# Performance work log

Measured on AMD Instinct MI355X. Metric: run time of the kernel, lower is better.

Reference implementation:

```python
import jax, jax.numpy as jnp
import numpy as np
from jax import lax

RO = 4.0            # snake_config.ro (feature-map downsample ratio)
N_ADJ = 4           # snake_config.adj_num -> kernel = 2*4+1 = 9
K = 2 * N_ADJ + 1
DIL = (1, 1, 1, 2, 2, 4, 4)   # dilations of the 7 Snake residual circular convs
NMS_RADIUS = 2      # radius used in the iterative refinement cls_nms


def circ_conv(x, w, b, d):
    """Dilated circular conv along polygon axis. x:[N,C,P], w:[O,I,K]."""
    pad = N_ADJ * d
    xp = jnp.concatenate([x[..., -pad:], x, x[..., :pad]], axis=-1)
    y = lax.conv_general_dilated(xp, w, window_strides=(1,), padding='VALID',
                                 rhs_dilation=(d,),
                                 dimension_numbers=('NCH', 'OIH', 'NCH'))
    return y + b[None, :, None]


def conv1x1(x, w, b):
    # x:[N,C,P], w:[O,C] -> [N,O,P]
    return jnp.einsum('ncp,oc->nop', x, w) + b[None, :, None]


def bilinear_gather(cnn_feature, poly, ind):
    """grid_sample-style bilinear sampling (align_corners=False, zero pad).
    cnn_feature:[B,C,H,W], poly:[N,P,2] pixel coords, ind:[N] image index.
    Returns [N,C,P]."""
    B, C, H, W = cnn_feature.shape
    x = poly[..., 0] - 0.5
    y = poly[..., 1] - 0.5
    x0 = jnp.floor(x); y0 = jnp.floor(y)
    wx = x - x0; wy = y - y0
    x0i = x0.astype(jnp.int32); y0i = y0.astype(jnp.int32)

    def tap(yi, xi):
        valid = (xi >= 0) & (xi < W) & (yi >= 0) & (yi < H)
        xi_c = jnp.clip(xi, 0, W - 1)
        yi_c = jnp.clip(yi, 0, H - 1)
        f = cnn_feature[ind[:, None], :, yi_c, xi_c]  # [N,P,C]
        return f * valid[..., None]

    f00 = tap(y0i, x0i);     f01 = tap(y0i, x0i + 1)
    f10 = tap(y0i + 1, x0i); f11 = tap(y0i + 1, x0i + 1)
    out = (f00 * ((1 - wx) * (1 - wy))[..., None]
           + f01 * (wx * (1 - wy))[..., None]
           + f10 * ((1 - wx) * wy)[..., None]
           + f11 * (wx * wy)[..., None])
    return out.transpose(0, 2, 1)  # [N,C,P]


def cls_nms(cls, radius):
    """Circular local-max suppression of per-vertex scores. cls:[N,P,1]."""
    c = cls[..., 0]
    m = jnp.max(jnp.stack([jnp.roll(c, s, axis=1)
                           for s in range(-radius, radius + 1)], 0), axis=0)
    return jnp.where(c >= m, c, 0.0)[..., None]


def snake_body(x, head_w, head_b, res_w, res_b, fusion_w, fusion_b,
               pred1_w, pred1_b, pred2_w, pred2_b, pred3_w, pred3_b,
               cls1_w, cls1_b, cls2_w, cls2_b, cls3_w, cls3_b):
    h = jax.nn.relu(circ_conv(x, head_w, head_b, 1))
    states = [h]
    for i in range(7):  # fixed 7 residual layers, structurally distinct dilations
        r = jax.nn.relu(circ_conv(states[-1], res_w[i], res_b[i], DIL[i]))
        states.append(r + states[-1])
    state = jnp.concatenate(states, axis=1)                 # [N, 8*128, P]
    g = conv1x1(state, fusion_w, fusion_b)                  # [N, 256, P]
    g = jnp.max(g, axis=2, keepdims=True)
    g = jnp.broadcast_to(g, (state.shape[0], g.shape[1], state.shape[2]))
    state = jnp.concatenate([g, state], axis=1)             # [N, 1280, P]

    def head3(w1, b1, w2, b2, w3, b3):
        h1 = jax.nn.relu(conv1x1(state, w1, b1))
        h2 = jax.nn.relu(conv1x1(h1, w2, b2))
        return conv1x1(h2, w3, b3)

    offset = head3(pred1_w, pred1_b, pred2_w, pred2_b, pred3_w, pred3_b)  # [N,2,P]
    cls = head3(cls1_w, cls1_b, cls2_w, cls2_b, cls3_w, cls3_b)           # [N,1,P]
    return offset, cls


def setup_inputs() -> dict:
    key = jax.random.key(0)
    ks = jax.random.split(key, 32)
    B, C, H, W = 4, 64, 128, 128
    N, P = 512, 128
    SD = 128  # state_dim
    FD = 64 + 2 + 1  # feature_dim for iterative evolve_gcn
    std = 0.01  # conv init: normal(0, 0.01), bias 0 (matches module init)
    inp = {
        'cnn_feature': jax.random.normal(ks[0], (B, C, H, W), jnp.float32),
        'i_it_py': jax.random.uniform(ks[1], (N, P, 2), jnp.float32) * (W - 1),
        'c_it_py': jax.random.normal(ks[2], (N, P, 2), jnp.float32) * 0.2,
        'it_cls': jax.random.uniform(ks[3], (N, P), jnp.float32),
        'ind': jax.random.randint(ks[4], (N,), 0, B, jnp.int32),
        'head_w': jax.random.normal(ks[5], (SD, FD, K), jnp.float32) * std,
        'head_b': jnp.zeros((SD,), jnp.float32),
        'res_w': jax.random.normal(ks[6], (7, SD, SD, K), jnp.float32) * std,
        'res_b': jnp.zeros((7, SD), jnp.float32),
        'fusion_w': jax.random.normal(ks[7], (256, 8 * SD), jnp.float32) * std,
        'fusion_b': jnp.zeros((256,), jnp.float32),
        'pred1_w': jax.random.normal(ks[8], (256, 8 * SD + 256), jnp.float32) * std,
        'pred1_b': jnp.zeros((256,), jnp.float32),
        'pred2_w': jax.random.normal(ks[9], (64, 256), jnp.float32) * std,
        'pred2_b': jnp.zeros((64,), jnp.float32),
        'pred3_w': jax.random.normal(ks[10], (2, 64), jnp.float32) * std,
        'pred3_b': jnp.zeros((2,), jnp.float32),
        'cls1_w': jax.random.normal(ks[11], (256, 8 * SD + 256), jnp.float32) * std,
        'cls1_b': jnp.zeros((256,), jnp.float32),
        'cls2_w': jax.random.normal(ks[12], (64, 256), jnp.float32) * std,
        'cls2_b': jnp.zeros((64,), jnp.float32),
        'cls3_w': jax.random.normal(ks[13], (1, 64), jnp.float32) * std,
        'cls3_b': jnp.zeros((1,), jnp.float32),
    }
    return inp


def reference(cnn_feature, i_it_py, c_it_py, it_cls, ind,
              head_w, head_b, res_w, res_b, fusion_w, fusion_b,
              pred1_w, pred1_b, pred2_w, pred2_b, pred3_w, pred3_b,
              cls1_w, cls1_b, cls2_w, cls2_b, cls3_w, cls3_b):
    # evolve_poly: gather CNN features at vertices, concat scaled canonical
    # coords + per-vertex cls, run Snake, add offsets, NMS sigmoid scores.
    feat = bilinear_gather(cnn_feature, i_it_py, ind)        # [N,64,P]
    c = (c_it_py * RO).transpose(0, 2, 1)                    # [N,2,P]
    x = jnp.concatenate([feat, c, it_cls[:, None, :]], axis=1)  # [N,67,P]
    offset, cls = snake_body(x, head_w, head_b, res_w, res_b, fusion_w, fusion_b,
                             pred1_w, pred1_b, pred2_w, pred2_b, pred3_w, pred3_b,
                             cls1_w, cls1_b, cls2_w, cls2_b, cls3_w, cls3_b)
    i_poly = i_it_py * RO + offset.transpose(0, 2, 1)        # [N,P,2]
    cls = cls.transpose(0, 2, 1)                             # [N,P,1]
    nms = cls_nms(jax.nn.sigmoid(cls), NMS_RADIUS)           # [N,P,1]
    return i_poly, cls, nms
```

## Files before the change

kernel.cpp:

```cpp
#include <hip/hip_runtime.h>
#include <math.h>

typedef __attribute__((ext_vector_type(8))) short bf16x8;
typedef __attribute__((ext_vector_type(4))) float f32x4;

#define UOFF_CAW 0L
#define UOFF_FAW 2359296L
#define UOFF_H1W 2883584L
#define UOFF_W2F 3932160L
#define NB_TOT   3997696L
#define OFF_W1G  1998848L
#define OFF_GRAW 2129920L
#define OFF_DYN  2260992L
#define REPACK_N 4128768L

__device__ inline ushort f2bf_rne(float x) {
  uint u = __float_as_uint(x);
  return (ushort)((u + 0x7FFFu + ((u >> 16) & 1u)) >> 16);
}
__device__ inline void split_bf(float x, ushort& h, ushort& l) {
  uint u = __float_as_uint(x);
  uint hb = (u + 0x7FFFu + ((u >> 16) & 1u)) & 0xFFFF0000u;
  h = (ushort)(hb >> 16);
  l = f2bf_rne(x - __uint_as_float(hb));
}
__device__ inline ushort bfsel(float w, int split) {
  uint u = __float_as_uint(w);
  uint hb = (u + 0x7FFFu + ((u >> 16) & 1u)) & 0xFFFF0000u;
  if (split == 0) return (ushort)(hb >> 16);
  float lo = w - __uint_as_float(hb);
  uint ul = __float_as_uint(lo);
  return (ushort)((ul + 0x7FFFu + ((ul >> 16) & 1u)) >> 16);
}
__device__ inline bf16x8 asb(uint4 a) {
  union { uint4 u; bf16x8 v; } x; x.u = a; return x.v;
}
__device__ inline f32x4 MFMA_(bf16x8 a, bf16x8 b, f32x4 c) {
  return __builtin_amdgcn_mfma_f32_16x16x32_bf16(a, b, c, 0, 0, 0);
}
__device__ inline void bar_lgkm() {
  asm volatile("s_waitcnt lgkmcnt(0)" ::: "memory");
  __builtin_amdgcn_s_barrier();
}

__device__ inline void read_frag_pair(const char* xb, int pc, int g, int ic,
                                      bf16x8& bh, bf16x8& bl) {
  const int s0 = (pc & 7) << 4;
  const char* a = xb + pc * 512 + (((ic * 64 + (g << 4))) ^ s0);
  bh = asb(*(const uint4*)a);
  bl = asb(*(const uint4*)(a + 256));
}

__global__ void k_repack(const float* __restrict__ head_w, const float* __restrict__ res_w,
                         const float* __restrict__ fusion_w,
                         const float* __restrict__ pred1_w, const float* __restrict__ cls1_w,
                         const float* __restrict__ pred2_w, const float* __restrict__ cls2_w,
                         float* __restrict__ ws) {
  const long j = (long)blockIdx.x * 256 + threadIdx.x;
  if (j >= REPACK_N) return;
  if (j < NB_TOT) {
    ushort* wsu = (ushort*)ws;
    float w;
    if (j < UOFF_FAW) {
      int e = (int)(j & 7); long q = j >> 3;
      int lane = (int)(q & 63); q >>= 6;
      int mt = (int)(q & 1); q >>= 1;
      int split = (int)(q & 1); q >>= 1;
      int ic = (int)(q & 3); q >>= 2;
      int tap = (int)(q % 9); q /= 9;
      int mp = (int)(q & 3); int l = (int)(q >> 2);
      int gg = lane >> 4;
      int kl = (e < 4) ? (4 * gg + e) : (16 + 4 * gg + e - 4);
      int m = mp * 32 + mt * 16 + (lane & 15);
      int i = ic * 32 + kl;
      if (l == 0) w = (i < 67) ? head_w[((long)m * 67 + i) * 9 + tap] : 0.f;
      else        w = res_w[(((long)(l - 1) * 128 + m) * 128 + i) * 9 + tap];
      wsu[j] = bfsel(w, split);
    } else if (j < UOFF_H1W) {
      long jj = j - UOFF_FAW;
      int e = (int)(jj & 7); long q = jj >> 3;
      int lane = (int)(q & 63); q >>= 6;
      int mt = (int)(q & 1); q >>= 1;
      int split = (int)(q & 1); q >>= 1;
      int ic = (int)(q & 3); q >>= 2;
      int fm2 = (int)(q & 7); int l = (int)(q >> 3);
      int gg = lane >> 4;
      int kl = (e < 4) ? (4 * gg + e) : (16 + 4 * gg + e - 4);
      int m = fm2 * 32 + mt * 16 + (lane & 15);
      int i = ic * 32 + kl;
      w = fusion_w[(long)m * 1024 + l * 128 + i];
      wsu[j] = bfsel(w, split);
    } else if (j < UOFF_W2F) {
      long jj = j - UOFF_H1W;
      int e = (int)(jj & 7); long q = jj >> 3;
      int lane = (int)(q & 63); q >>= 6;
      int mt = (int)(q & 1); q >>= 1;
      int split = (int)(q & 1); q >>= 1;
      int ic = (int)(q & 3); q >>= 2;
      int slab = (int)(q & 7); q >>= 3;
      int mp = (int)(q & 7); int blk = (int)(q >> 3);
      int gg = lane >> 4;
      int kl = (e < 4) ? (4 * gg + e) : (16 + 4 * gg + e - 4);
      int m = blk * 256 + mp * 32 + mt * 16 + (lane & 15);
      int k = slab * 128 + ic * 32 + kl;
      w = (m < 256) ? pred1_w[(long)m * 1280 + 256 + k] : cls1_w[(long)(m - 256) * 1280 + 256 + k];
      wsu[j] = bfsel(w, split);
    } else {
      long jj = j - UOFF_W2F;
      int e = (int)(jj & 7); long q = jj >> 3;
      int lane = (int)(q & 63); q >>= 6;
      int split = (int)(q & 1); q >>= 1;
      int ic = (int)(q & 7); q >>= 3;
      int mfr = (int)(q & 3); int blk = (int)(q >> 2);
      int gg = lane >> 4;
      int kl = (e < 4) ? (4 * gg + e) : (16 + 4 * gg + e - 4);
      int m = mfr * 16 + (lane & 15);
      int k = ic * 32 + kl;
      w = blk ? cls2_w[(long)m * 256 + k] : pred2_w[(long)m * 256 + k];
      wsu[j] = bfsel(w, split);
    }
  } else {
    long q = j - NB_TOT; int o = (int)(q & 511); int c = (int)(q >> 9);
    ws[OFF_W1G + q] = (o < 256) ? pred1_w[(long)o * 1280 + c] : cls1_w[(long)(o - 256) * 1280 + c];
  }
}

__global__ __launch_bounds__(1024) __attribute__((amdgpu_waves_per_eu(4)))
void k_conv(const float* __restrict__ cnn, const float* __restrict__ i_it,
            const float* __restrict__ c_it, const float* __restrict__ cls_in,
            const int* __restrict__ ind,
            const ushort* __restrict__ CAW, const ushort* __restrict__ FAW,
            const float* __restrict__ head_b, const float* __restrict__ res_b,
            float* __restrict__ graw, float* __restrict__ states, int p0) {
  __shared__ uint4 xt4[4096];
  __shared__ float scr[512];
  char* xb = (char*)xt4;
  const int ln = blockIdx.x, n = p0 + ln, t = threadIdx.x;
  const int lane = t & 63, li = lane & 15, g = lane >> 4;
  const int wv = __builtin_amdgcn_readfirstlane(t >> 6);
  const int mp = wv & 3, np = wv >> 2;
  const int fm2 = wv & 7, fq = wv >> 3;

  {
    const int p = t & 127, qg = t >> 7;
    const long nb = (long)n * 128 + p;
    const int sw = p & 7;
    if (qg < 4) {
      const float gx = i_it[nb * 2 + 0] - 0.5f;
      const float gy = i_it[nb * 2 + 1] - 0.5f;
      const float fx = floorf(gx), fy = floorf(gy);
      const float wx = gx - fx, wy = gy - fy;
      const int x0 = (int)fx, y0 = (int)fy, x1 = x0 + 1, y1 = y0 + 1;
      const bool vx0 = (x0 >= 0) & (x0 < 128), vx1 = (x1 >= 0) & (x1 < 128);
      const bool vy0 = (y0 >= 0) & (y0 < 128), vy1 = (y1 >= 0) & (y1 < 128);
      const int x0c = min(max(x0, 0), 127), x1c = min(max(x1, 0), 127);
      const int y0c = min(max(y0, 0), 127), y1c = min(max(y1, 0), 127);
      const float w00 = (vx0 && vy0) ? (1.f - wx) * (1.f - wy) : 0.f;
      const float w01 = (vx1 && vy0) ? wx * (1.f - wy) : 0.f;
      const float w10 = (vx0 && vy1) ? (1.f - wx) * wy : 0.f;
      const float w11 = (vx1 && vy1) ? wx * wy : 0.f;
      const long base = (long)ind[n] * (64L * 16384);
      const int a00 = y0c * 128 + x0c, a01 = y0c * 128 + x1c;
      const int a10 = y1c * 128 + x0c, a11 = y1c * 128 + x1c;
#pragma unroll
      for (int qq = 0; qq < 4; qq++) {
        ushort hh[4], ll[4];
#pragma unroll
        for (int cc = 0; cc < 4; cc++) {
          const int c = qg * 16 + qq * 4 + cc;
          const float* f = cnn + base + (long)c * 16384;
          float x = f[a00] * w00 + f[a01] * w01 + f[a10] * w10 + f[a11] * w11;
          split_bf(x, hh[cc], ll[cc]);
        }
        const int G = ((qg >> 1) * 4 + qq) ^ sw;
        char* a = xb + p * 512 + G * 16 + (qg & 1) * 8;
        *(uint2*)a = make_uint2((uint)hh[0] | ((uint)hh[1] << 16), (uint)hh[2] | ((uint)hh[3] << 16));
        *(uint2*)(a + 256) = make_uint2((uint)ll[0] | ((uint)ll[1] << 16), (uint)ll[2] | ((uint)ll[3] << 16));
      }
    } else {
#pragma unroll
      for (int qq = 0; qq < 4; qq++) {
        ushort hh[4], ll[4];
        if (qg == 4 && qq == 0) {
          float v0 = c_it[nb * 2 + 0] * 4.f, v1 = c_it[nb * 2 + 1] * 4.f, v2 = cls_in[nb];
          split_bf(v0, hh[0], ll[0]); split_bf(v1, hh[1], ll[1]); split_bf(v2, hh[2], ll[2]);
          hh[3] = 0; ll[3] = 0;
        } else {
          hh[0] = hh[1] = hh[2] = hh[3] = 0; ll[0] = ll[1] = ll[2] = ll[3] = 0;
        }
        const int G = ((qg >> 1) * 4 + qq) ^ sw;
        char* a = xb + p * 512 + G * 16 + (qg & 1) * 8;
        *(uint2*)a = make_uint2((uint)hh[0] | ((uint)hh[1] << 16), (uint)hh[2] | ((uint)hh[3] << 16));
        *(uint2*)(a + 256) = make_uint2((uint)ll[0] | ((uint)ll[1] << 16), (uint)ll[2] | ((uint)ll[3] << 16));
      }
    }
  }
  __syncthreads();

  const f32x4 fz = {0.f, 0.f, 0.f, 0.f};
  f32x4 facc[2][4];
#pragma unroll
  for (int a = 0; a < 2; a++)
#pragma unroll
    for (int b = 0; b < 4; b++) facc[a][b] = fz;

  const uint4* caw = (const uint4*)CAW;
  const uint4* faw = (const uint4*)FAW;
  uint4* stq = (uint4*)(states + (long)ln * 131072);

  for (int l = 0; l < 8; l++) {
    const int dil = (l >= 6) ? 4 : ((l >= 4) ? 2 : 1);
    const int nic = (l == 0) ? 3 : 4;
    if (l > 0) {
      uint4* dst = stq + (long)(l - 1) * 4096;
#pragma unroll
      for (int k = 0; k < 4; k++) dst[k * 1024 + t] = xt4[k * 1024 + t];
      const uint4* fawl = faw + ((long)((l - 1) * 8 + fm2)) * 1024 + lane;
#pragma unroll
      for (int ic = 0; ic < 4; ic++) {
        const uint4* w0 = fawl + ic * 256;
        const bf16x8 Ah0 = asb(w0[0]),   Ah1 = asb(w0[64]);
        const bf16x8 Al0 = asb(w0[128]), Al1 = asb(w0[192]);
#pragma unroll
        for (int nt = 0; nt < 4; nt++) {
          const int pc = fq * 64 + nt * 16 + li;
          bf16x8 bh, bl;
          read_frag_pair(xb, pc, g, ic, bh, bl);
          facc[0][nt] = MFMA_(Ah0, bh, facc[0][nt]);
          facc[1][nt] = MFMA_(Ah1, bh, facc[1][nt]);
          facc[0][nt] = MFMA_(Ah0, bl, facc[0][nt]);
          facc[1][nt] = MFMA_(Ah1, bl, facc[1][nt]);
          facc[0][nt] = MFMA_(Al0, bh, facc[0][nt]);
          facc[1][nt] = MFMA_(Al1, bh, facc[1][nt]);
        }
      }
    }
    f32x4 cacc[2][2];
    cacc[0][0] = fz; cacc[0][1] = fz; cacc[1][0] = fz; cacc[1][1] = fz;
    const uint4* cawl = caw + ((long)(l * 4 + mp)) * 9216;
    for (int tap = 0; tap < 9; tap++) {
      const int shift = (tap - 4) * dil;
      const int pc0 = (np * 32 + li + shift + 128) & 127;
      const int pc1 = (np * 32 + 16 + li + shift + 128) & 127;
      const uint4* cawt = cawl + tap * 1024 + lane;
      for (int ic = 0; ic < nic; ic++) {
        bf16x8 bh0, bl0, bh1, bl1;
        read_frag_pair(xb, pc0, g, ic, bh0, bl0);
        read_frag_pair(xb, pc1, g, ic, bh1, bl1);
        const uint4* w0 = cawt + ic * 256;
        const bf16x8 Ah0 = asb(w0[0]),   Ah1 = asb(w0[64]);
        const bf16x8 Al0 = asb(w0[128]), Al1 = asb(w0[192]);
        cacc[0][0] = MFMA_(Ah0, bh0, cacc[0][0]);
        cacc[0][1] = MFMA_(Ah0, bh1, cacc[0][1]);
        cacc[1][0] = MFMA_(Ah1, bh0, cacc[1][0]);
        cacc[1][1] = MFMA_(Ah1, bh1, cacc[1][1]);
        cacc[0][0] = MFMA_(Ah0, bl0, cacc[0][0]);
        cacc[0][1] = MFMA_(Ah0, bl1, cacc[0][1]);
        cacc[1][0] = MFMA_(Ah1, bl0, cacc[1][0]);
        cacc[1][1] = MFMA_(Ah1, bl1, cacc[1][1]);
        cacc[0][0] = MFMA_(Al0, bh0, cacc[0][0]);
        cacc[0][1] = MFMA_(Al0, bh1, cacc[0][1]);
        cacc[1][0] = MFMA_(Al1, bh0, cacc[1][0]);
        cacc[1][1] = MFMA_(Al1, bh1, cacc[1][1]);
      }
    }
    bar_lgkm();
    {
      const float* bsrc = (l == 0) ? head_b : (res_b + (l - 1) * 128);
      const float4 b0 = *(const float4*)&bsrc[mp * 32 + g * 4];
      const float4 b1 = *(const float4*)&bsrc[mp * 32 + 16 + g * 4];
#pragma unroll
      for (int nt = 0; nt < 2; nt++) {
        const int p = np * 32 + nt * 16 + li;
        const int X = (mp * 64 + g * 16) ^ ((p & 7) << 4);
        char* a = xb + p * 512 + X;
        float v[8];
        v[0] = fmaxf(cacc[0][nt][0] + b0.x, 0.f);
        v[1] = fmaxf(cacc[0][nt][1] + b0.y, 0.f);
        v[2] = fmaxf(cacc[0][nt][2] + b0.z, 0.f);
        v[3] = fmaxf(cacc[0][nt][3] + b0.w, 0.f);
        v[4] = fmaxf(cacc[1][nt][0] + b1.x, 0.f);
        v[5] = fmaxf(cacc[1][nt][1] + b1.y, 0.f);
        v[6] = fmaxf(cacc[1][nt][2] + b1.z, 0.f);
        v[7] = fmaxf(cacc[1][nt][3] + b1.w, 0.f);
        if (l > 0) {
          const uint4 oh = *(const uint4*)a;
          const uint4 ol = *(const uint4*)(a + 256);
          const uint hw[4] = {oh.x, oh.y, oh.z, oh.w};
          const uint lw[4] = {ol.x, ol.y, ol.z, ol.w};
#pragma unroll
          for (int k = 0; k < 8; k++) {
            const uint hh = (k & 1) ? (hw[k >> 1] & 0xFFFF0000u) : ((hw[k >> 1] & 0xFFFFu) << 16);
            const uint ll = (k & 1) ? (lw[k >> 1] & 0xFFFF0000u) : ((lw[k >> 1] & 0xFFFFu) << 16);
            v[k] += __uint_as_float(hh) + __uint_as_float(ll);
          }
        }
        ushort hh[8], ll[8];
#pragma unroll
        for (int k = 0; k < 8; k++) split_bf(v[k], hh[k], ll[k]);
        *(uint4*)a = make_uint4((uint)hh[0] | ((uint)hh[1] << 16), (uint)hh[2] | ((uint)hh[3] << 16),
                                (uint)hh[4] | ((uint)hh[5] << 16), (uint)hh[6] | ((uint)hh[7] << 16));
        *(uint4*)(a + 256) = make_uint4((uint)ll[0] | ((uint)ll[1] << 16), (uint)ll[2] | ((uint)ll[3] << 16),
                                        (uint)ll[4] | ((uint)ll[5] << 16), (uint)ll[6] | ((uint)ll[7] << 16));
      }
    }
    __syncthreads();
  }

  {
    uint4* dst = stq + 7L * 4096;
#pragma unroll
    for (int k = 0; k < 4; k++) dst[k * 1024 + t] = xt4[k * 1024 + t];
    const uint4* fawl = faw + ((long)(7 * 8 + fm2)) * 1024 + lane;
#pragma unroll
    for (int ic = 0; ic < 4; ic++) {
      const uint4* w0 = fawl + ic * 256;
      const bf16x8 Ah0 = asb(w0[0]),   Ah1 = asb(w0[64]);
      const bf16x8 Al0 = asb(w0[128]), Al1 = asb(w0[192]);
#pragma unroll
      for (int nt = 0; nt < 4; nt++) {
        const int pc = fq * 64 + nt * 16 + li;
        bf16x8 bh, bl;
        read_frag_pair(xb, pc, g, ic, bh, bl);
        facc[0][nt] = MFMA_(Ah0, bh, facc[0][nt]);
        facc[1][nt] = MFMA_(Ah1, bh, facc[1][nt]);
        facc[0][nt] = MFMA_(Ah0, bl, facc[0][nt]);
        facc[1][nt] = MFMA_(Ah1, bl, facc[1][nt]);
        facc[0][nt] = MFMA_(Al0, bh, facc[0][nt]);
        facc[1][nt] = MFMA_(Al1, bh, facc[1][nt]);
      }
    }
  }

#pragma unroll
  for (int mt = 0; mt < 2; mt++) {
#pragma unroll
    for (int r = 0; r < 4; r++) {
      float m = fmaxf(fmaxf(facc[mt][0][r], facc[mt][1][r]),
                      fmaxf(facc[mt][2][r], facc[mt][3][r]));
#pragma unroll
      for (int s = 1; s < 16; s <<= 1) m = fmaxf(m, __shfl_xor(m, s, 64));
      if (li == 0) scr[(fm2 * 32 + mt * 16 + g * 4 + r) * 2 + fq] = m;
    }
  }
  bar_lgkm();
  if (t < 256) graw[(long)n * 256 + t] = fmaxf(scr[2 * t], scr[2 * t + 1]);
}

__global__ __launch_bounds__(1024) __attribute__((amdgpu_waves_per_eu(4)))
void k_h1t(const float* __restrict__ states, const ushort* __restrict__ H1W,
           const ushort* __restrict__ W2F,
           const float* __restrict__ graw, const float* __restrict__ fus_b,
           const float* __restrict__ W1G, const float* __restrict__ p1b, const float* __restrict__ c1b,
           const float* __restrict__ p2b, const float* __restrict__ c2b,
           float* __restrict__ h2, int p0) {
  __shared__ uint4 xt4[4096];
  __shared__ float sg[256];
  __shared__ float hg_s[256];
  char* xb = (char*)xt4;
  const int b = blockIdx.x, ln = b >> 1, blk = b & 1, t = threadIdx.x;
  const int n = p0 + ln;
  const int lane = t & 63, li = lane & 15, g = lane >> 4;
  const int wv = __builtin_amdgcn_readfirstlane(t >> 6);
  const int mw = wv & 7, qw = wv >> 3;
  const uint4* sp = (const uint4*)(states + (long)ln * 131072);
  const uint4* aw = (const uint4*)H1W;
  const uint4* w2 = (const uint4*)W2F;
  const f32x4 fz = {0.f, 0.f, 0.f, 0.f};

  uint4 stg[4];
#pragma unroll
  for (int k = 0; k < 4; k++) stg[k] = sp[k * 1024 + t];

  if (t < 256) sg[t] = graw[(long)n * 256 + t] + fus_b[t];
  __syncthreads();
  if (t < 256) {
    float s = blk ? c1b[t] : p1b[t];
    const float* w = W1G + blk * 256 + t;
#pragma unroll 8
    for (int c = 0; c < 256; c++) s = fmaf(w[(long)c * 512], sg[c], s);
    hg_s[t] = s;
  }

  f32x4 acc[2][4];
#pragma unroll
  for (int a = 0; a < 2; a++)
#pragma unroll
    for (int c = 0; c < 4; c++) acc[a][c] = fz;

  for (int s = 0; s < 8; s++) {
#pragma unroll
    for (int k = 0; k < 4; k++) xt4[k * 1024 + t] = stg[k];
    bar_lgkm();
    if (s < 7) {
#pragma unroll
      for (int k = 0; k < 4; k++) stg[k] = sp[(s + 1) * 4096 + k * 1024 + t];
    }
    const uint4* awl = aw + (((long)(blk * 8 + mw)) * 8 + s) * 1024 + lane;
#pragma unroll
    for (int ic = 0; ic < 4; ic++) {
      const uint4* w0 = awl + ic * 256;
      const bf16x8 Ah0 = asb(w0[0]),   Ah1 = asb(w0[64]);
      const bf16x8 Al0 = asb(w0[128]), Al1 = asb(w0[192]);
#pragma unroll
      for (int nt = 0; nt < 4; nt++) {
        const int pc = qw * 64 + nt * 16 + li;
        bf16x8 bh, bl;
        read_frag_pair(xb, pc, g, ic, bh, bl);
        acc[0][nt] = MFMA_(Ah0, bh, acc[0][nt]);
        acc[1][nt] = MFMA_(Ah1, bh, acc[1][nt]);
        acc[0][nt] = MFMA_(Ah0, bl, acc[0][nt]);
        acc[1][nt] = MFMA_(Ah1, bl, acc[1][nt]);
        acc[0][nt] = MFMA_(Al0, bh, acc[0][nt]);
        acc[1][nt] = MFMA_(Al1, bh, acc[1][nt]);
      }
    }
    bar_lgkm();
  }

  const float4 hq0 = *(const float4*)&hg_s[mw * 32 + g * 4];
  const float4 hq1 = *(const float4*)&hg_s[mw * 32 + 16 + g * 4];
#pragma unroll
  for (int nt = 0; nt < 4; nt++) {
    acc[0][nt][0] = fmaxf(acc[0][nt][0] + hq0.x, 0.f);
    acc[0][nt][1] = fmaxf(acc[0][nt][1] + hq0.y, 0.f);
    acc[0][nt][2] = fmaxf(acc[0][nt][2] + hq0.z, 0.f);
    acc[0][nt][3] = fmaxf(acc[0][nt][3] + hq0.w, 0.f);
    acc[1][nt][0] = fmaxf(acc[1][nt][0] + hq1.x, 0.f);
    acc[1][nt][1] = fmaxf(acc[1][nt][1] + hq1.y, 0.f);
    acc[1][nt][2] = fmaxf(acc[1][nt][2] + hq1.z, 0.f);
    acc[1][nt][3] = fmaxf(acc[1][nt][3] + hq1.w, 0.f);
  }

  const int mfr = wv & 3, nfr = wv >> 2;
  const float* b2 = blk ? c2b : p2b;
  float* hbase = h2 + (long)ln * 16384;
  for (int h = 0; h < 2; h++) {
    bar_lgkm();
    if (qw == h) {
#pragma unroll
      for (int nt = 0; nt < 4; nt++) {
        const int pl = nt * 16 + li;
        char* a = xb + pl * 1024 + ((mw * 64 + g * 16) ^ ((pl & 7) << 4));
        ushort hh[8], ll[8];
#pragma unroll
        for (int e = 0; e < 4; e++) { split_bf(acc[0][nt][e], hh[e], ll[e]); }
#pragma unroll
        for (int e = 0; e < 4; e++) { split_bf(acc[1][nt][e], hh[4 + e], ll[4 + e]); }
        *(uint4*)a = make_uint4((uint)hh[0] | ((uint)hh[1] << 16), (uint)hh[2] | ((uint)hh[3] << 16),
                                (uint)hh[4] | ((uint)hh[5] << 16), (uint)hh[6] | ((uint)hh[7] << 16));
        *(uint4*)(a + 512) = make_uint4((uint)ll[0] | ((uint)ll[1] << 16), (uint)ll[2] | ((uint)ll[3] << 16),
                                        (uint)ll[4] | ((uint)ll[5] << 16), (uint)ll[6] | ((uint)ll[7] << 16));
      }
    }
    bar_lgkm();
    f32x4 a2 = fz;
#pragma unroll
    for (int ic = 0; ic < 8; ic++) {
      const uint4* wb = w2 + (((long)(blk * 4 + mfr) * 8 + ic) * 2) * 64 + lane;
      const bf16x8 Ah = asb(wb[0]), Al = asb(wb[64]);
      const int pl = nfr * 16 + li;
      const char* ba = xb + pl * 1024 + ((ic * 64 + g * 16) ^ ((pl & 7) << 4));
      const bf16x8 bh = asb(*(const uint4*)ba);
      const bf16x8 bl = asb(*(const uint4*)(ba + 512));
      a2 = MFMA_(Ah, bh, a2);
      a2 = MFMA_(Ah, bl, a2);
      a2 = MFMA_(Al, bh, a2);
    }
    const int jl = mfr * 16 + g * 4;
    float* hout = hbase + (long)(blk * 64 + jl) * 128 + h * 64 + nfr * 16 + li;
    hout[0]   = fmaxf(a2[0] + b2[jl + 0], 0.f);
    hout[128] = fmaxf(a2[1] + b2[jl + 1], 0.f);
    hout[256] = fmaxf(a2[2] + b2[jl + 2], 0.f);
    hout[384] = fmaxf(a2[3] + b2[jl + 3], 0.f);
  }
}

__global__ __launch_bounds__(128)
void k_tail2(const float* __restrict__ h2,
             const float* __restrict__ p3w, const float* __restrict__ p3b,
             const float* __restrict__ c3w, const float* __restrict__ c3b,
             const float* __restrict__ i_it, float* __restrict__ out, int p0) {
  __shared__ float sb[128];
  const int ln = blockIdx.x, n = p0 + ln, pp = threadIdx.x;
  const float* hp = h2 + (long)ln * 16384;
  float o0v = p3b[0], o1v = p3b[1], cv = c3b[0];
  for (int j = 0; j < 64; j++) {
    const float hpx = hp[j * 128 + pp];
    const float hcx = hp[(64 + j) * 128 + pp];
    o0v = fmaf(p3w[j], hpx, o0v);
    o1v = fmaf(p3w[64 + j], hpx, o1v);
    cv = fmaf(c3w[j], hcx, cv);
  }
  const long ip = ((long)n * 128 + pp) * 2;
  out[ip + 0] = i_it[ip + 0] * 4.f + o0v;
  out[ip + 1] = i_it[ip + 1] * 4.f + o1v;
  out[131072 + (long)n * 128 + pp] = cv;
  const float sig = 1.f / (1.f + expf(-cv));
  sb[pp] = sig;
  __syncthreads();
  float m = sb[pp];
#pragma unroll
  for (int s = 1; s <= 2; s++) {
    m = fmaxf(m, sb[(pp + s) & 127]);
    m = fmaxf(m, sb[(pp + 128 - s) & 127]);
  }
  out[196608 + (long)n * 128 + pp] = (sig >= m) ? sig : 0.f;
}

extern "C" void kernel_launch(void* const* d_in, const int* in_sizes, int n_in,
                              void* d_out, int out_size, void* d_ws, size_t ws_size,
                              hipStream_t stream) {
  const float* cnn      = (const float*)d_in[0];
  const float* i_it     = (const float*)d_in[1];
  const float* c_it     = (const float*)d_in[2];
  const float* it_cls   = (const float*)d_in[3];
  const int*   ind      = (const int*)d_in[4];
  const float* head_w   = (const float*)d_in[5];
  const float* head_b   = (const float*)d_in[6];
  const float* res_w    = (const float*)d_in[7];
  const float* res_b    = (const float*)d_in[8];
  const float* fusion_w = (const float*)d_in[9];
  const float* fusion_b = (const float*)d_in[10];
  const float* pred1_w  = (const float*)d_in[11];
  const float* pred1_b  = (const float*)d_in[12];
  const float* pred2_w  = (const float*)d_in[13];
  const float* pred2_b  = (const float*)d_in[14];
  const float* pred3_w  = (const float*)d_in[15];
  const float* pred3_b  = (const float*)d_in[16];
  const float* cls1_w   = (const float*)d_in[17];
  const float* cls1_b   = (const float*)d_in[18];
  const float* cls2_w   = (const float*)d_in[19];
  const float* cls2_b   = (const float*)d_in[20];
  const float* cls3_w   = (const float*)d_in[21];
  const float* cls3_b   = (const float*)d_in[22];
  float* ws = (float*)d_ws;
  float* out = (float*)d_out;
  const ushort* wsu = (const ushort*)d_ws;

  k_repack<<<(int)((REPACK_N + 255) / 256), 256, 0, stream>>>(
      head_w, res_w, fusion_w, pred1_w, cls1_w, pred2_w, cls2_w, ws);

  long avail_f = (long)(ws_size / 4) - OFF_DYN;
  long Cl = avail_f / 147456;
  int C = (Cl >= 512) ? 512 : ((Cl >= 256) ? 256 : (int)(Cl < 1 ? 1 : Cl));
  float* states = ws + OFF_DYN;
  float* h2 = states + (long)C * 131072;

  for (int p0 = 0; p0 < 512; p0 += C) {
    int Cc = (512 - p0 < C) ? (512 - p0) : C;
    k_conv<<<Cc, 1024, 0, stream>>>(cnn, i_it, c_it, it_cls, ind,
                                    wsu + UOFF_CAW, wsu + UOFF_FAW, head_b, res_b,
                                    ws + OFF_GRAW, states, p0);
    k_h1t<<<2 * Cc, 1024, 0, stream>>>(states, wsu + UOFF_H1W, wsu + UOFF_W2F,
                                       ws + OFF_GRAW, fusion_b, ws + OFF_W1G,
                                       pred1_b, cls1_b, pred2_b, cls2_b, h2, p0);
    k_tail2<<<Cc, 128, 0, stream>>>(h2, pred3_w, pred3_b, cls3_w, cls3_b,
                                    i_it, out, p0);
  }
}
```

Measured before the change: 976.4 us.

## Fuse Snake conv, prediction head, and tail into one per-polygon kernel

Merges the conv kernel, the two-block head kernel (pred1/cls1 and pred2/cls2), and the tail kernel into a single kernel with one block per polygon. The final layer state now stays in LDS instead of going through global memory, and the global-max vector, the h2 intermediate and two launches are removed. Each block now computes both pred and cls branches (four M-fragments per wave instead of two). This halves the grid of the head stage and raises register pressure, which may reduce parallelism.

```diff
diff --git a/kernel.cpp b/kernel.cpp
--- a/kernel.cpp
+++ b/kernel.cpp
@@ -10,8 +10,7 @@
 #define UOFF_W2F 3932160L
 #define NB_TOT   3997696L
 #define OFF_W1G  1998848L
-#define OFF_GRAW 2129920L
-#define OFF_DYN  2260992L
+#define OFF_DYN  2129920L
 #define REPACK_N 4128768L
 
 __device__ inline ushort f2bf_rne(float x) {
@@ -126,20 +125,29 @@
 }
 
 __global__ __launch_bounds__(1024) __attribute__((amdgpu_waves_per_eu(4)))
-void k_conv(const float* __restrict__ cnn, const float* __restrict__ i_it,
-            const float* __restrict__ c_it, const float* __restrict__ cls_in,
-            const int* __restrict__ ind,
-            const ushort* __restrict__ CAW, const ushort* __restrict__ FAW,
-            const float* __restrict__ head_b, const float* __restrict__ res_b,
-            float* __restrict__ graw, float* __restrict__ states, int p0) {
+void k_fused(const float* __restrict__ cnn, const float* __restrict__ i_it,
+             const float* __restrict__ c_it, const float* __restrict__ cls_in,
+             const int* __restrict__ ind,
+             const ushort* __restrict__ CAW, const ushort* __restrict__ FAW,
+             const ushort* __restrict__ H1W, const ushort* __restrict__ W2F,
+             const float* __restrict__ head_b, const float* __restrict__ res_b,
+             const float* __restrict__ fus_b, const float* __restrict__ W1G,
+             const float* __restrict__ p1b, const float* __restrict__ c1b,
+             const float* __restrict__ p2b, const float* __restrict__ c2b,
+             const float* __restrict__ p3w, const float* __restrict__ p3b,
+             const float* __restrict__ c3w, const float* __restrict__ c3b,
+             float* __restrict__ states, float* __restrict__ out, int p0) {
   __shared__ uint4 xt4[4096];
   __shared__ float scr[512];
+  __shared__ float sg[256];
+  __shared__ float hg_s[512];
   char* xb = (char*)xt4;
   const int ln = blockIdx.x, n = p0 + ln, t = threadIdx.x;
   const int lane = t & 63, li = lane & 15, g = lane >> 4;
   const int wv = __builtin_amdgcn_readfirstlane(t >> 6);
   const int mp = wv & 3, np = wv >> 2;
   const int fm2 = wv & 7, fq = wv >> 3;
+  const int mw = wv & 7, qw = wv >> 3;
 
   {
     const int p = t & 127, qg = t >> 7;
@@ -206,7 +214,7 @@
 
   const uint4* caw = (const uint4*)CAW;
   const uint4* faw = (const uint4*)FAW;
-  uint4* stq = (uint4*)(states + (long)ln * 131072);
+  uint4* stq = (uint4*)(states + (long)ln * 114688);
 
   for (int l = 0; l < 8; l++) {
     const int dil = (l >= 6) ? 4 : ((l >= 4) ? 2 : 1);
@@ -308,9 +316,6 @@
   }
 
   {
-    uint4* dst = stq + 7L * 4096;
-#pragma unroll
-    for (int k = 0; k < 4; k++) dst[k * 1024 + t] = xt4[k * 1024 + t];
     const uint4* fawl = faw + ((long)(7 * 8 + fm2)) * 1024 + lane;
 #pragma unroll
     for (int ic = 0; ic < 4; ic++) {
@@ -343,169 +348,199 @@
       if (li == 0) scr[(fm2 * 32 + mt * 16 + g * 4 + r) * 2 + fq] = m;
     }
   }
+  asm volatile("s_waitcnt vmcnt(0)" ::: "memory");
   bar_lgkm();
-  if (t < 256) graw[(long)n * 256 + t] = fmaxf(scr[2 * t], scr[2 * t + 1]);
-}
-
-__global__ __launch_bounds__(1024) __attribute__((amdgpu_waves_per_eu(4)))
-void k_h1t(const float* __restrict__ states, const ushort* __restrict__ H1W,
-           const ushort* __restrict__ W2F,
-           const float* __restrict__ graw, const float* __restrict__ fus_b,
-           const float* __restrict__ W1G, const float* __restrict__ p1b, const float* __restrict__ c1b,
-           const float* __restrict__ p2b, const float* __restrict__ c2b,
-           float* __restrict__ h2, int p0) {
-  __shared__ uint4 xt4[4096];
-  __shared__ float sg[256];
-  __shared__ float hg_s[256];
-  char* xb = (char*)xt4;
-  const int b = blockIdx.x, ln = b >> 1, blk = b & 1, t = threadIdx.x;
-  const int n = p0 + ln;
-  const int lane = t & 63, li = lane & 15, g = lane >> 4;
-  const int wv = __builtin_amdgcn_readfirstlane(t >> 6);
-  const int mw = wv & 7, qw = wv >> 3;
-  const uint4* sp = (const uint4*)(states + (long)ln * 131072);
-  const uint4* aw = (const uint4*)H1W;
-  const uint4* w2 = (const uint4*)W2F;
-  const f32x4 fz = {0.f, 0.f, 0.f, 0.f};
-
+  if (t < 256) sg[t] = fmaxf(scr[2 * t], scr[2 * t + 1]) + fus_b[t];
+
+  const uint4* sp = (const uint4*)stq;
   uint4 stg[4];
 #pragma unroll
   for (int k = 0; k < 4; k++) stg[k] = sp[k * 1024 + t];
-
-  if (t < 256) sg[t] = graw[(long)n * 256 + t] + fus_b[t];
-  __syncthreads();
-  if (t < 256) {
-    float s = blk ? c1b[t] : p1b[t];
-    const float* w = W1G + blk * 256 + t;
+  bar_lgkm();
+
+  if (t < 512) {
+    float s = (t < 256) ? p1b[t] : c1b[t - 256];
+    const float* w = W1G + t;
 #pragma unroll 8
     for (int c = 0; c < 256; c++) s = fmaf(w[(long)c * 512], sg[c], s);
     hg_s[t] = s;
   }
 
-  f32x4 acc[2][4];
-#pragma unroll
-  for (int a = 0; a < 2; a++)
-#pragma unroll
-    for (int c = 0; c < 4; c++) acc[a][c] = fz;
-
-  for (int s = 0; s < 8; s++) {
+  const uint4* aw = (const uint4*)H1W;
+  f32x4 hacc[4][4];
+#pragma unroll
+  for (int f = 0; f < 4; f++)
+#pragma unroll
+    for (int c = 0; c < 4; c++) hacc[f][c] = fz;
+
+#pragma unroll
+  for (int ic = 0; ic < 4; ic++) {
+    const uint4* w00 = aw + ((long)((2 * mw + 0) * 8 + 7)) * 1024 + ic * 256 + lane;
+    const uint4* w01 = aw + ((long)((2 * mw + 1) * 8 + 7)) * 1024 + ic * 256 + lane;
+    const bf16x8 Ah0 = asb(w00[0]),   Ah1 = asb(w00[64]);
+    const bf16x8 Al0 = asb(w00[128]), Al1 = asb(w00[192]);
+    const bf16x8 Ah2 = asb(w01[0]),   Ah3 = asb(w01[64]);
+    const bf16x8 Al2 = asb(w01[128]), Al3 = asb(w01[192]);
+#pragma unroll
+    for (int nt = 0; nt < 4; nt++) {
+      const int pc = qw * 64 + nt * 16 + li;
+      bf16x8 bh, bl;
+      read_frag_pair(xb, pc, g, ic, bh, bl);
+      hacc[0][nt] = MFMA_(Ah0, bh, hacc[0][nt]);
+      hacc[1][nt] = MFMA_(Ah1, bh, hacc[1][nt]);
+      hacc[2][nt] = MFMA_(Ah2, bh, hacc[2][nt]);
+      hacc[3][nt] = MFMA_(Ah3, bh, hacc[3][nt]);
+      hacc[0][nt] = MFMA_(Ah0, bl, hacc[0][nt]);
+      hacc[1][nt] = MFMA_(Ah1, bl, hacc[1][nt]);
+      hacc[2][nt] = MFMA_(Ah2, bl, hacc[2][nt]);
+      hacc[3][nt] = MFMA_(Ah3, bl, hacc[3][nt]);
+      hacc[0][nt] = MFMA_(Al0, bh, hacc[0][nt]);
+      hacc[1][nt] = MFMA_(Al1, bh, hacc[1][nt]);
+      hacc[2][nt] = MFMA_(Al2, bh, hacc[2][nt]);
+      hacc[3][nt] = MFMA_(Al3, bh, hacc[3][nt]);
+    }
+  }
+  for (int s = 0; s < 7; s++) {
+    bar_lgkm();
 #pragma unroll
     for (int k = 0; k < 4; k++) xt4[k * 1024 + t] = stg[k];
     bar_lgkm();
-    if (s < 7) {
-#pragma unroll
-      for (int k = 0; k < 4; k++) stg[k] = sp[(s + 1) * 4096 + k * 1024 + t];
-    }
-    const uint4* awl = aw + (((long)(blk * 8 + mw)) * 8 + s) * 1024 + lane;
+    if (s < 6) {
+#pragma unroll
+      for (int k = 0; k < 4; k++) stg[k] = sp[(long)(s + 1) * 4096 + k * 1024 + t];
+    }
 #pragma unroll
     for (int ic = 0; ic < 4; ic++) {
-      const uint4* w0 = awl + ic * 256;
-      const bf16x8 Ah0 = asb(w0[0]),   Ah1 = asb(w0[64]);
-      const bf16x8 Al0 = asb(w0[128]), Al1 = asb(w0[192]);
+      const uint4* w00 = aw + ((long)((2 * mw + 0) * 8 + s)) * 1024 + ic * 256 + lane;
+      const uint4* w01 = aw + ((long)((2 * mw + 1) * 8 + s)) * 1024 + ic * 256 + lane;
+      const bf16x8 Ah0 = asb(w00[0]),   Ah1 = asb(w00[64]);
+      const bf16x8 Al0 = asb(w00[128]), Al1 = asb(w00[192]);
+      const bf16x8 Ah2 = asb(w01[0]),   Ah3 = asb(w01[64]);
+      const bf16x8 Al2 = asb(w01[128]), Al3 = asb(w01[192]);
 #pragma unroll
       for (int nt = 0; nt < 4; nt++) {
         const int pc = qw * 64 + nt * 16 + li;
         bf16x8 bh, bl;
         read_frag_pair(xb, pc, g, ic, bh, bl);
-        acc[0][nt] = MFMA_(Ah0, bh, acc[0][nt]);
-        acc[1][nt] = MFMA_(Ah1, bh, acc[1][nt]);
-        acc[0][nt] = MFMA_(Ah0, bl, acc[0][nt]);
-        acc[1][nt] = MFMA_(Ah1, bl, acc[1][nt]);
-        acc[0][nt] = MFMA_(Al0, bh, acc[0][nt]);
-        acc[1][nt] = MFMA_(Al1, bh, acc[1][nt]);
+        hacc[0][nt] = MFMA_(Ah0, bh, hacc[0][nt]);
+        hacc[1][nt] = MFMA_(Ah1, bh, hacc[1][nt]);
+        hacc[2][nt] = MFMA_(Ah2, bh, hacc[2][nt]);
+        hacc[3][nt] = MFMA_(Ah3, bh, hacc[3][nt]);
+        hacc[0][nt] = MFMA_(Ah0, bl, hacc[0][nt]);
+        hacc[1][nt] = MFMA_(Ah1, bl, hacc[1][nt]);
+        hacc[2][nt] = MFMA_(Ah2, bl, hacc[2][nt]);
+        hacc[3][nt] = MFMA_(Ah3, bl, hacc[3][nt]);
+        hacc[0][nt] = MFMA_(Al0, bh, hacc[0][nt]);
+        hacc[1][nt] = MFMA_(Al1, bh, hacc[1][nt]);
+        hacc[2][nt] = MFMA_(Al2, bh, hacc[2][nt]);
+        hacc[3][nt] = MFMA_(Al3, bh, hacc[3][nt]);
+      }
+    }
+  }
+  bar_lgkm();
+
+#pragma unroll
+  for (int f = 0; f < 4; f++) {
+    const float4 hq = *(const float4*)&hg_s[mw * 64 + f * 16 + g * 4];
+#pragma unroll
+    for (int nt = 0; nt < 4; nt++) {
+      hacc[f][nt][0] = fmaxf(hacc[f][nt][0] + hq.x, 0.f);
+      hacc[f][nt][1] = fmaxf(hacc[f][nt][1] + hq.y, 0.f);
+      hacc[f][nt][2] = fmaxf(hacc[f][nt][2] + hq.z, 0.f);
+      hacc[f][nt][3] = fmaxf(hacc[f][nt][3] + hq.w, 0.f);
+    }
+  }
+
+  const uint4* w2 = (const uint4*)W2F;
+  f32x4 a2q[4];
+  for (int q = 0; q < 4; q++) {
+    a2q[q] = fz;
+    if (qw == (q >> 1)) {
+#pragma unroll
+      for (int fp = 0; fp < 4; fp += 2) {
+        const int kc = 2 * mw + (fp >> 1);
+#pragma unroll
+        for (int ntl = 0; ntl < 2; ntl++) {
+          const int nt = 2 * (q & 1) + ntl;
+          const int pl = ntl * 16 + li;
+          char* a = xb + pl * 2048 + ((kc * 64 + g * 16) ^ ((pl & 7) << 4));
+          ushort hh[8], ll[8];
+#pragma unroll
+          for (int e = 0; e < 4; e++) { split_bf(hacc[fp][nt][e], hh[e], ll[e]); }
+#pragma unroll
+          for (int e = 0; e < 4; e++) { split_bf(hacc[fp + 1][nt][e], hh[4 + e], ll[4 + e]); }
+          *(uint4*)a = make_uint4((uint)hh[0] | ((uint)hh[1] << 16), (uint)hh[2] | ((uint)hh[3] << 16),
+                                  (uint)hh[4] | ((uint)hh[5] << 16), (uint)hh[6] | ((uint)hh[7] << 16));
+          *(uint4*)(a + 1024) = make_uint4((uint)ll[0] | ((uint)ll[1] << 16), (uint)ll[2] | ((uint)ll[3] << 16),
+                                           (uint)ll[4] | ((uint)ll[5] << 16), (uint)ll[6] | ((uint)ll[7] << 16));
+        }
       }
     }
     bar_lgkm();
-  }
-
-  const float4 hq0 = *(const float4*)&hg_s[mw * 32 + g * 4];
-  const float4 hq1 = *(const float4*)&hg_s[mw * 32 + 16 + g * 4];
-#pragma unroll
-  for (int nt = 0; nt < 4; nt++) {
-    acc[0][nt][0] = fmaxf(acc[0][nt][0] + hq0.x, 0.f);
-    acc[0][nt][1] = fmaxf(acc[0][nt][1] + hq0.y, 0.f);
-    acc[0][nt][2] = fmaxf(acc[0][nt][2] + hq0.z, 0.f);
-    acc[0][nt][3] = fmaxf(acc[0][nt][3] + hq0.w, 0.f);
-    acc[1][nt][0] = fmaxf(acc[1][nt][0] + hq1.x, 0.f);
-    acc[1][nt][1] = fmaxf(acc[1][nt][1] + hq1.y, 0.f);
-    acc[1][nt][2] = fmaxf(acc[1][nt][2] + hq1.z, 0.f);
-    acc[1][nt][3] = fmaxf(acc[1][nt][3] + hq1.w, 0.f);
-  }
-
-  const int mfr = wv & 3, nfr = wv >> 2;
-  const float* b2 = blk ? c2b : p2b;
-  float* hbase = h2 + (long)ln * 16384;
-  for (int h = 0; h < 2; h++) {
+    {
+      const int blkc = mw >> 2;
+      const int pl = qw * 16 + li;
+#pragma unroll
+      for (int ic8 = 0; ic8 < 8; ic8++) {
+        const int kc = blkc * 8 + ic8;
+        const uint4* wb = w2 + (((long)(blkc * 4 + (mw & 3)) * 8 + ic8) * 2) * 64 + lane;
+        const bf16x8 Ah = asb(wb[0]), Al = asb(wb[64]);
+        const char* ba = xb + pl * 2048 + ((kc * 64 + g * 16) ^ ((pl & 7) << 4));
+        const bf16x8 bh = asb(*(const uint4*)ba);
+        const bf16x8 bl = asb(*(const uint4*)(ba + 1024));
+        a2q[q] = MFMA_(Ah, bh, a2q[q]);
+        a2q[q] = MFMA_(Ah, bl, a2q[q]);
+        a2q[q] = MFMA_(Al, bh, a2q[q]);
+      }
+    }
     bar_lgkm();
-    if (qw == h) {
-#pragma unroll
-      for (int nt = 0; nt < 4; nt++) {
-        const int pl = nt * 16 + li;
-        char* a = xb + pl * 1024 + ((mw * 64 + g * 16) ^ ((pl & 7) << 4));
-        ushort hh[8], ll[8];
-#pragma unroll
-        for (int e = 0; e < 4; e++) { split_bf(acc[0][nt][e], hh[e], ll[e]); }
-#pragma unroll
-        for (int e = 0; e < 4; e++) { split_bf(acc[1][nt][e], hh[4 + e], ll[4 + e]); }
-        *(uint4*)a = make_uint4((uint)hh[0] | ((uint)hh[1] << 16), (uint)hh[2] | ((uint)hh[3] << 16),
-                                (uint)hh[4] | ((uint)hh[5] << 16), (uint)hh[6] | ((uint)hh[7] << 16));
-        *(uint4*)(a + 512) = make_uint4((uint)ll[0] | ((uint)ll[1] << 16), (uint)ll[2] | ((uint)ll[3] << 16),
-                                        (uint)ll[4] | ((uint)ll[5] << 16), (uint)ll[6] | ((uint)ll[7] << 16));
-      }
+  }
+
+  {
+    float* h2L = (float*)xb;
+#pragma unroll
+    for (int q = 0; q < 4; q++) {
+#pragma unroll
+      for (int e = 0; e < 4; e++) {
+        const int row = mw * 16 + g * 4 + e;
+        const float bb = (mw < 4) ? p2b[row] : c2b[row - 64];
+        h2L[row * 128 + q * 32 + qw * 16 + li] = fmaxf(a2q[q][e] + bb, 0.f);
+      }
+    }
+  }
+  bar_lgkm();
+
+  {
+    const float* h2L = (const float*)xb;
+    float sig = 0.f;
+    const int pp = t & 127;
+    if (t < 128) {
+      float o0v = p3b[0], o1v = p3b[1], cv = c3b[0];
+      for (int j = 0; j < 64; j++) {
+        const float hp = h2L[j * 128 + pp];
+        const float hc = h2L[(64 + j) * 128 + pp];
+        o0v = fmaf(p3w[j], hp, o0v);
+        o1v = fmaf(p3w[64 + j], hp, o1v);
+        cv = fmaf(c3w[j], hc, cv);
+      }
+      const long ip = ((long)n * 128 + pp) * 2;
+      out[ip + 0] = i_it[ip + 0] * 4.f + o0v;
+      out[ip + 1] = i_it[ip + 1] * 4.f + o1v;
+      out[131072 + (long)n * 128 + pp] = cv;
+      sig = 1.f / (1.f + expf(-cv));
+      scr[pp] = sig;
     }
     bar_lgkm();
-    f32x4 a2 = fz;
-#pragma unroll
-    for (int ic = 0; ic < 8; ic++) {
-      const uint4* wb = w2 + (((long)(blk * 4 + mfr) * 8 + ic) * 2) * 64 + lane;
-      const bf16x8 Ah = asb(wb[0]), Al = asb(wb[64]);
-      const int pl = nfr * 16 + li;
-      const char* ba = xb + pl * 1024 + ((ic * 64 + g * 16) ^ ((pl & 7) << 4));
-      const bf16x8 bh = asb(*(const uint4*)ba);
-      const bf16x8 bl = asb(*(const uint4*)(ba + 512));
-      a2 = MFMA_(Ah, bh, a2);
-      a2 = MFMA_(Ah, bl, a2);
-      a2 = MFMA_(Al, bh, a2);
-    }
-    const int jl = mfr * 16 + g * 4;
-    float* hout = hbase + (long)(blk * 64 + jl) * 128 + h * 64 + nfr * 16 + li;
-    hout[0]   = fmaxf(a2[0] + b2[jl + 0], 0.f);
-    hout[128] = fmaxf(a2[1] + b2[jl + 1], 0.f);
-    hout[256] = fmaxf(a2[2] + b2[jl + 2], 0.f);
-    hout[384] = fmaxf(a2[3] + b2[jl + 3], 0.f);
-  }
-}
-
-__global__ __launch_bounds__(128)
-void k_tail2(const float* __restrict__ h2,
-             const float* __restrict__ p3w, const float* __restrict__ p3b,
-             const float* __restrict__ c3w, const float* __restrict__ c3b,
-             const float* __restrict__ i_it, float* __restrict__ out, int p0) {
-  __shared__ float sb[128];
-  const int ln = blockIdx.x, n = p0 + ln, pp = threadIdx.x;
-  const float* hp = h2 + (long)ln * 16384;
-  float o0v = p3b[0], o1v = p3b[1], cv = c3b[0];
-  for (int j = 0; j < 64; j++) {
-    const float hpx = hp[j * 128 + pp];
-    const float hcx = hp[(64 + j) * 128 + pp];
-    o0v = fmaf(p3w[j], hpx, o0v);
-    o1v = fmaf(p3w[64 + j], hpx, o1v);
-    cv = fmaf(c3w[j], hcx, cv);
-  }
-  const long ip = ((long)n * 128 + pp) * 2;
-  out[ip + 0] = i_it[ip + 0] * 4.f + o0v;
-  out[ip + 1] = i_it[ip + 1] * 4.f + o1v;
-  out[131072 + (long)n * 128 + pp] = cv;
-  const float sig = 1.f / (1.f + expf(-cv));
-  sb[pp] = sig;
-  __syncthreads();
-  float m = sb[pp];
-#pragma unroll
-  for (int s = 1; s <= 2; s++) {
-    m = fmaxf(m, sb[(pp + s) & 127]);
-    m = fmaxf(m, sb[(pp + 128 - s) & 127]);
-  }
-  out[196608 + (long)n * 128 + pp] = (sig >= m) ? sig : 0.f;
+    if (t < 128) {
+      float m = scr[pp];
+#pragma unroll
+      for (int s = 1; s <= 2; s++) {
+        m = fmaxf(m, scr[(pp + s) & 127]);
+        m = fmaxf(m, scr[(pp + 128 - s) & 127]);
+      }
+      out[196608 + (long)n * 128 + pp] = (sig >= m) ? sig : 0.f;
+    }
+  }
 }
 
 extern "C" void kernel_launch(void* const* d_in, const int* in_sizes, int n_in,
@@ -542,20 +577,18 @@
       head_w, res_w, fusion_w, pred1_w, cls1_w, pred2_w, cls2_w, ws);
 
   long avail_f = (long)(ws_size / 4) - OFF_DYN;
-  long Cl = avail_f / 147456;
+  long Cl = avail_f / 114688;
   int C = (Cl >= 512) ? 512 : ((Cl >= 256) ? 256 : (int)(Cl < 1 ? 1 : Cl));
   float* states = ws + OFF_DYN;
-  float* h2 = states + (long)C * 131072;
 
   for (int p0 = 0; p0 < 512; p0 += C) {
     int Cc = (512 - p0 < C) ? (512 - p0) : C;
-    k_conv<<<Cc, 1024, 0, stream>>>(cnn, i_it, c_it, it_cls, ind,
-                                    wsu + UOFF_CAW, wsu + UOFF_FAW, head_b, res_b,
-                                    ws + OFF_GRAW, states, p0);
-    k_h1t<<<2 * Cc, 1024, 0, stream>>>(states, wsu + UOFF_H1W, wsu + UOFF_W2F,
-                                       ws + OFF_GRAW, fusion_b, ws + OFF_W1G,
-                                       pred1_b, cls1_b, pred2_b, cls2_b, h2, p0);
-    k_tail2<<<Cc, 128, 0, stream>>>(h2, pred3_w, pred3_b, cls3_w, cls3_b,
-                                    i_it, out, p0);
-  }
-}
+    k_fused<<<Cc, 1024, 0, stream>>>(cnn, i_it, c_it, it_cls, ind,
+                                     wsu + UOFF_CAW, wsu + UOFF_FAW,
+                                     wsu + UOFF_H1W, wsu + UOFF_W2F,
+                                     head_b, res_b, fusion_b, ws + OFF_W1G,
+                                     pred1_b, cls1_b, pred2_b, cls2_b,
+                                     pred3_w, pred3_b, cls3_w, cls3_b,
+                                     states, out, p0);
+  }
+}
```

New measurement: 1.033 ms. +5.8%, slower.

## Fuse tail prediction/cls/NMS stage into k_h1t via shared-memory h2

Applied to the files above, without the earlier changes.

Stops k_h1t from writing the second hidden layer to global workspace. The result now stays in LDS, and the final pred3/cls3 projections, sigmoid and circular NMS run inside the same block, so the separate k_tail2 launch is gone. This removes one kernel launch per chunk and a global write/read round trip of h2. The cost is a few extra barriers and a tail phase where only 128 of 1024 threads are active. The reduced workspace need may also allow larger chunks.

```diff
diff --git a/kernel.cpp b/kernel.cpp
--- a/kernel.cpp
+++ b/kernel.cpp
@@ -353,7 +353,9 @@
            const float* __restrict__ graw, const float* __restrict__ fus_b,
            const float* __restrict__ W1G, const float* __restrict__ p1b, const float* __restrict__ c1b,
            const float* __restrict__ p2b, const float* __restrict__ c2b,
-           float* __restrict__ h2, int p0) {
+           const float* __restrict__ p3w, const float* __restrict__ p3b,
+           const float* __restrict__ c3w, const float* __restrict__ c3b,
+           const float* __restrict__ i_it, float* __restrict__ out, int p0) {
   __shared__ uint4 xt4[4096];
   __shared__ float sg[256];
   __shared__ float hg_s[256];
@@ -434,7 +436,8 @@
 
   const int mfr = wv & 3, nfr = wv >> 2;
   const float* b2 = blk ? c2b : p2b;
-  float* hbase = h2 + (long)ln * 16384;
+  f32x4 a2s[2];
+#pragma unroll
   for (int h = 0; h < 2; h++) {
     bar_lgkm();
     if (qw == h) {
@@ -454,58 +457,74 @@
       }
     }
     bar_lgkm();
-    f32x4 a2 = fz;
-#pragma unroll
-    for (int ic = 0; ic < 8; ic++) {
-      const uint4* wb = w2 + (((long)(blk * 4 + mfr) * 8 + ic) * 2) * 64 + lane;
-      const bf16x8 Ah = asb(wb[0]), Al = asb(wb[64]);
+    a2s[h] = fz;
+    {
       const int pl = nfr * 16 + li;
-      const char* ba = xb + pl * 1024 + ((ic * 64 + g * 16) ^ ((pl & 7) << 4));
-      const bf16x8 bh = asb(*(const uint4*)ba);
-      const bf16x8 bl = asb(*(const uint4*)(ba + 512));
-      a2 = MFMA_(Ah, bh, a2);
-      a2 = MFMA_(Ah, bl, a2);
-      a2 = MFMA_(Al, bh, a2);
-    }
+#pragma unroll
+      for (int ic = 0; ic < 8; ic++) {
+        const uint4* wb = w2 + (((long)(blk * 4 + mfr) * 8 + ic) * 2) * 64 + lane;
+        const bf16x8 Ah = asb(wb[0]), Al = asb(wb[64]);
+        const char* ba = xb + pl * 1024 + ((ic * 64 + g * 16) ^ ((pl & 7) << 4));
+        const bf16x8 bh = asb(*(const uint4*)ba);
+        const bf16x8 bl = asb(*(const uint4*)(ba + 512));
+        a2s[h] = MFMA_(Ah, bh, a2s[h]);
+        a2s[h] = MFMA_(Ah, bl, a2s[h]);
+        a2s[h] = MFMA_(Al, bh, a2s[h]);
+      }
+    }
+  }
+  bar_lgkm();
+
+  {
+    float* h2L = (float*)xb;
     const int jl = mfr * 16 + g * 4;
-    float* hout = hbase + (long)(blk * 64 + jl) * 128 + h * 64 + nfr * 16 + li;
-    hout[0]   = fmaxf(a2[0] + b2[jl + 0], 0.f);
-    hout[128] = fmaxf(a2[1] + b2[jl + 1], 0.f);
-    hout[256] = fmaxf(a2[2] + b2[jl + 2], 0.f);
-    hout[384] = fmaxf(a2[3] + b2[jl + 3], 0.f);
-  }
-}
-
-__global__ __launch_bounds__(128)
-void k_tail2(const float* __restrict__ h2,
-             const float* __restrict__ p3w, const float* __restrict__ p3b,
-             const float* __restrict__ c3w, const float* __restrict__ c3b,
-             const float* __restrict__ i_it, float* __restrict__ out, int p0) {
-  __shared__ float sb[128];
-  const int ln = blockIdx.x, n = p0 + ln, pp = threadIdx.x;
-  const float* hp = h2 + (long)ln * 16384;
-  float o0v = p3b[0], o1v = p3b[1], cv = c3b[0];
-  for (int j = 0; j < 64; j++) {
-    const float hpx = hp[j * 128 + pp];
-    const float hcx = hp[(64 + j) * 128 + pp];
-    o0v = fmaf(p3w[j], hpx, o0v);
-    o1v = fmaf(p3w[64 + j], hpx, o1v);
-    cv = fmaf(c3w[j], hcx, cv);
-  }
-  const long ip = ((long)n * 128 + pp) * 2;
-  out[ip + 0] = i_it[ip + 0] * 4.f + o0v;
-  out[ip + 1] = i_it[ip + 1] * 4.f + o1v;
-  out[131072 + (long)n * 128 + pp] = cv;
-  const float sig = 1.f / (1.f + expf(-cv));
-  sb[pp] = sig;
-  __syncthreads();
-  float m = sb[pp];
-#pragma unroll
-  for (int s = 1; s <= 2; s++) {
-    m = fmaxf(m, sb[(pp + s) & 127]);
-    m = fmaxf(m, sb[(pp + 128 - s) & 127]);
-  }
-  out[196608 + (long)n * 128 + pp] = (sig >= m) ? sig : 0.f;
+#pragma unroll
+    for (int h = 0; h < 2; h++) {
+      const int pos = h * 64 + nfr * 16 + li;
+      h2L[(jl + 0) * 128 + pos] = fmaxf(a2s[h][0] + b2[jl + 0], 0.f);
+      h2L[(jl + 1) * 128 + pos] = fmaxf(a2s[h][1] + b2[jl + 1], 0.f);
+      h2L[(jl + 2) * 128 + pos] = fmaxf(a2s[h][2] + b2[jl + 2], 0.f);
+      h2L[(jl + 3) * 128 + pos] = fmaxf(a2s[h][3] + b2[jl + 3], 0.f);
+    }
+  }
+  bar_lgkm();
+
+  {
+    const float* h2L = (const float*)xb;
+    const int pp = t & 127;
+    if (blk == 0) {
+      if (t < 128) {
+        float o0v = p3b[0], o1v = p3b[1];
+        for (int j = 0; j < 64; j++) {
+          const float hp = h2L[j * 128 + pp];
+          o0v = fmaf(p3w[j], hp, o0v);
+          o1v = fmaf(p3w[64 + j], hp, o1v);
+        }
+        const long ip = ((long)n * 128 + pp) * 2;
+        out[ip + 0] = i_it[ip + 0] * 4.f + o0v;
+        out[ip + 1] = i_it[ip + 1] * 4.f + o1v;
+      }
+    } else {
+      float sig = 0.f;
+      if (t < 128) {
+        float cv = c3b[0];
+        for (int j = 0; j < 64; j++) cv = fmaf(c3w[j], h2L[j * 128 + pp], cv);
+        out[131072 + (long)n * 128 + pp] = cv;
+        sig = 1.f / (1.f + expf(-cv));
+        sg[pp] = sig;
+      }
+      bar_lgkm();
+      if (t < 128) {
+        float m = sg[pp];
+#pragma unroll
+        for (int s = 1; s <= 2; s++) {
+          m = fmaxf(m, sg[(pp + s) & 127]);
+          m = fmaxf(m, sg[(pp + 128 - s) & 127]);
+        }
+        out[196608 + (long)n * 128 + pp] = (sig >= m) ? sig : 0.f;
+      }
+    }
+  }
 }
 
 extern "C" void kernel_launch(void* const* d_in, const int* in_sizes, int n_in,
@@ -542,10 +561,9 @@
       head_w, res_w, fusion_w, pred1_w, cls1_w, pred2_w, cls2_w, ws);
 
   long avail_f = (long)(ws_size / 4) - OFF_DYN;
-  long Cl = avail_f / 147456;
+  long Cl = avail_f / 131072;
   int C = (Cl >= 512) ? 512 : ((Cl >= 256) ? 256 : (int)(Cl < 1 ? 1 : Cl));
   float* states = ws + OFF_DYN;
-  float* h2 = states + (long)C * 131072;
 
   for (int p0 = 0; p0 < 512; p0 += C) {
     int Cc = (512 - p0 < C) ? (512 - p0) : C;
@@ -554,8 +572,8 @@
                                     ws + OFF_GRAW, states, p0);
     k_h1t<<<2 * Cc, 1024, 0, stream>>>(states, wsu + UOFF_H1W, wsu + UOFF_W2F,
                                        ws + OFF_GRAW, fusion_b, ws + OFF_W1G,
-                                       pred1_b, cls1_b, pred2_b, cls2_b, h2, p0);
-    k_tail2<<<Cc, 128, 0, stream>>>(h2, pred3_w, pred3_b, cls3_w, cls3_b,
-                                    i_it, out, p0);
-  }
-}
+                                       pred1_b, cls1_b, pred2_b, cls2_b,
+                                       pred3_w, pred3_b, cls3_w, cls3_b,
+                                       i_it, out, p0);
+  }
+}
```

Measured after the change: 1.022 ms. +4.6%, slower.
